# Kernel optimization log

Hardware: AMD Instinct MI355X
Metric: run time of the kernel (lower is better)

The kernel has to match this reference:

```python
import jax, jax.numpy as jnp
import numpy as np

B, C, H, W = 8, 512, 64, 64
KD, VD, OD = 64, 512, 512
BN_EPS = 1e-5


def setup_inputs() -> dict:
    key = jax.random.key(0)
    ks = jax.random.split(key, 10)
    s = lambda fan_in: 1.0 / np.sqrt(fan_in)
    return {
        "x": jax.random.normal(ks[0], (B, C, H, W), jnp.float32),
        "Wq": jax.random.normal(ks[1], (KD, C), jnp.float32) * s(C),
        "bq": jnp.zeros((KD,), jnp.float32),
        "Wk": jax.random.normal(ks[2], (KD, C), jnp.float32) * s(C),
        "bk": jnp.zeros((KD,), jnp.float32),
        "Wv": jax.random.normal(ks[3], (VD, C), jnp.float32) * s(C),
        "bv": jnp.zeros((VD,), jnp.float32),
        "gamma": jnp.zeros((1,), jnp.float32),  # torch init: zeros(1)
        "Wf": jax.random.normal(ks[4], (OD, VD), jnp.float32) * s(VD),
        "bn_w": jnp.ones((OD,), jnp.float32),
        "bn_b": jnp.zeros((OD,), jnp.float32),
        "bn_mean": jnp.zeros((OD,), jnp.float32),
        "bn_var": jnp.ones((OD,), jnp.float32),
    }


def reference(x, Wq, bq, Wk, bk, Wv, bv, gamma, Wf, bn_w, bn_b, bn_mean, bn_var):
    b, c, h, w = x.shape
    n = h * w
    # 1x1 convs == per-pixel channel matmuls
    q = jnp.einsum('bchw,kc->bkhw', x, Wq) + bq[None, :, None, None]  # [B,KD,H,W]
    k = jnp.einsum('bchw,kc->bkhw', x, Wk) + bk[None, :, None, None]
    v = jnp.einsum('bchw,vc->bvhw', x, Wv) + bv[None, :, None, None]
    q = q.reshape(b, -1, n)  # [B,KD,N]
    k = k.reshape(b, -1, n)
    v = v.reshape(b, -1, n)  # [B,VD,N]
    # energy[b, i, j] = q[:, :, i] . k[:, :, j]   (proj_query permuted)
    energy = jnp.einsum('bki,bkj->bij', q, k)  # [B,N,N]
    attention = jax.nn.softmax(energy, axis=-1)
    # out = value @ attention^T : out[b, v, i] = sum_j value[b, v, j] * attention[b, i, j]
    out = jnp.einsum('bvj,bij->bvi', v, attention)  # [B,VD,N]
    out = out.reshape(b, c, h, w)
    out = gamma * out + x
    # fuse: 1x1 conv (no bias) -> BatchNorm (inference) -> ReLU
    fused = jnp.einsum('bchw,oc->bohw', out, Wf)
    inv = jax.lax.rsqrt(bn_var + BN_EPS)
    fused = (fused - bn_mean[None, :, None, None]) * (bn_w * inv)[None, :, None, None] + bn_b[None, :, None, None]
    return jax.nn.relu(fused)
```

## Files before the change

### kernel.cpp

```cpp
#include <hip/hip_runtime.h>
#include <hip/hip_bf16.h>

typedef unsigned short u16;
typedef unsigned int u32;
typedef __attribute__((ext_vector_type(8))) short bf16x8;
typedef __attribute__((ext_vector_type(4))) float f32x4;
typedef __attribute__((ext_vector_type(4))) u16 u16x4;

#define B_ 8
#define C_ 512
#define N_ 4096
#define KD_ 64
#define VD_ 512
#define OD_ 512

static __device__ __forceinline__ float bf2f(u16 u) {
    union { u32 i; float f; } z; z.i = ((u32)u) << 16; return z.f;
}
static __device__ __forceinline__ u16 f2bf(float f) {
    union { float f; u32 u; } v; v.f = f;
    u32 r = v.u + 0x7fffu + ((v.u >> 16) & 1u);
    return (u16)(r >> 16);
}
static __device__ __forceinline__ u32 pkbf(float lo, float hi) {
    u32 ul = __float_as_uint(lo) + 0x8000u;
    u32 uh = __float_as_uint(hi) + 0x8000u;
    return __builtin_amdgcn_perm(uh, ul, 0x07060302u);
}
static __device__ __forceinline__ int swz(int row) { return ((row >> 2) + (row >> 4)) & 3; }

static __device__ __forceinline__ void tile_barrier() {
    asm volatile("s_waitcnt lgkmcnt(0)" ::: "memory");
    __builtin_amdgcn_s_barrier();
    asm volatile("" ::: "memory");
}

__global__ __launch_bounds__(256) void transpose_convert_kernel(
    const float* __restrict__ x, const float* __restrict__ Wf,
    const float* __restrict__ gamma,
    u16* __restrict__ xT, u16* __restrict__ Wf16)
{
    const int t = threadIdx.x;
    if (blockIdx.x >= 256) {
        const int tid = (blockIdx.x - 256) * 256 + t;
        const float4* src = (const float4*)Wf + (size_t)tid * 16;
        u16* dst = Wf16 + (size_t)tid * 64;
        #pragma unroll
        for (int j = 0; j < 16; j++) {
            const float4 f = src[j];
            u16x4 p;
            p[0] = f2bf(f.x); p[1] = f2bf(f.y); p[2] = f2bf(f.z); p[3] = f2bf(f.w);
            *(u16x4*)(dst + j * 4) = p;
        }
        return;
    }
    if (gamma[0] == 0.0f) return;
    __shared__ u32 tile[64][33];
    for (int it = 0; it < 16; it++) {
        const int bid = it * 256 + blockIdx.x;
        const int nt = bid & 63;
        const int ct = (bid >> 6) & 7;
        const int b  = bid >> 9;
        const float* xb  = x  + ((size_t)b * C_ + ct * 64) * N_ + nt * 64;
        u16*         xTb = xT + ((size_t)b * N_ + nt * 64) * C_ + ct * 64;
        {
            const int p  = t >> 3;
            const int n8 = t & 7;
            const float* r0 = xb + (size_t)(2 * p)     * N_ + n8 * 8;
            const float* r1 = xb + (size_t)(2 * p + 1) * N_ + n8 * 8;
            const float4 a0 = *(const float4*)(r0);
            const float4 a1 = *(const float4*)(r0 + 4);
            const float4 c0 = *(const float4*)(r1);
            const float4 c1 = *(const float4*)(r1 + 4);
            const float av[8] = { a0.x, a0.y, a0.z, a0.w, a1.x, a1.y, a1.z, a1.w };
            const float cv[8] = { c0.x, c0.y, c0.z, c0.w, c1.x, c1.y, c1.z, c1.w };
            #pragma unroll
            for (int j = 0; j < 8; j++)
                tile[n8 * 8 + j][p] = (u32)f2bf(av[j]) | ((u32)f2bf(cv[j]) << 16);
        }
        __syncthreads();
        #pragma unroll
        for (int h = 0; h < 2; h++) {
            const int id = t + h * 256;
            const int n  = id >> 3;
            const int q  = id & 7;
            uint4 val;
            val.x = tile[n][q * 4 + 0];
            val.y = tile[n][q * 4 + 1];
            val.z = tile[n][q * 4 + 2];
            val.w = tile[n][q * 4 + 3];
            *(uint4*)(xTb + (size_t)n * C_ + q * 8) = val;
        }
        __syncthreads();
    }
}

__global__ __launch_bounds__(256) void proj_kernel(
    const u16* __restrict__ xT,
    const float* __restrict__ Wq, const float* __restrict__ bq,
    const float* __restrict__ Wk, const float* __restrict__ bk,
    const float* __restrict__ Wv, const float* __restrict__ bv,
    const float* __restrict__ gamma,
    u16* __restrict__ q, u16* __restrict__ k, u16* __restrict__ v)
{
    if (gamma[0] == 0.0f) return;
    for (int it = 0; it < 2; it++) {
        const int bid = it * 256 + blockIdx.x;
        const int b = bid >> 6;
        const int p = (bid & 63) * 64 + (threadIdx.x & 63);
        const int dg = threadIdx.x >> 6;
        const u16* xrow = xT + ((size_t)b * N_ + p) * C_;
        for (int d0 = dg * 160; d0 < dg * 160 + 160; d0++) {
            const float* wrow; float bias; u16* dst; int dd; int dim;
            if (d0 < 64)       { dd = d0;       wrow = Wq + (size_t)dd * C_; bias = bq[dd]; dst = q; dim = KD_; }
            else if (d0 < 128) { dd = d0 - 64;  wrow = Wk + (size_t)dd * C_; bias = bk[dd]; dst = k; dim = KD_; }
            else               { dd = d0 - 128; wrow = Wv + (size_t)dd * C_; bias = bv[dd]; dst = v; dim = VD_; }
            float s = bias;
            for (int c = 0; c < C_; c++) s += bf2f(xrow[c]) * wrow[c];
            dst[((size_t)b * dim + dd) * N_ + p] = f2bf(s);
        }
    }
}

__global__ __launch_bounds__(256) void attn_kernel(
    const u16* __restrict__ xT, const u16* __restrict__ q,
    const u16* __restrict__ k, const u16* __restrict__ v,
    const float* __restrict__ gamma, u16* __restrict__ yT)
{
    const float g = gamma[0];
    if (g == 0.0f) return;
    __shared__ float pls[4][64];
    const int wv = threadIdx.x >> 6, lane = threadIdx.x & 63;
    for (int it = 0; it < 4; it++) {
        const int bid = it * 256 + blockIdx.x;
        const int b  = bid >> 7;
        const int q0 = (bid & 127) * 32 + wv * 8;
        const u16* kb = k + (size_t)b * KD_ * N_;
        const u16* vb = v + (size_t)b * VD_ * N_;
        for (int qi = 0; qi < 8; qi++) {
            const int i = q0 + qi;
            const float qv = bf2f(q[((size_t)b * KD_ + lane) * N_ + i]);
            float mx = -1e30f, l = 0.f;
            for (int jb = 0; jb < N_; jb += 64) {
                float e = 0.f;
                for (int kd = 0; kd < 64; kd++)
                    e += __shfl(qv, kd) * bf2f(kb[(size_t)kd * N_ + jb + lane]);
                const float nm = fmaxf(mx, e);
                l = l * __expf(mx - nm) + __expf(e - nm);
                mx = nm;
            }
            for (int off = 32; off; off >>= 1) {
                const float mo = __shfl_xor(mx, off);
                const float lo = __shfl_xor(l, off);
                const float nm = fmaxf(mx, mo);
                l = l * __expf(mx - nm) + lo * __expf(mo - nm);
                mx = nm;
            }
            float oacc[8];
            #pragma unroll
            for (int r = 0; r < 8; r++) oacc[r] = 0.f;
            for (int jb = 0; jb < N_; jb += 64) {
                float e = 0.f;
                for (int kd = 0; kd < 64; kd++)
                    e += __shfl(qv, kd) * bf2f(kb[(size_t)kd * N_ + jb + lane]);
                __syncthreads();
                pls[wv][lane] = __expf(e - mx);
                __syncthreads();
                for (int jj = 0; jj < 64; jj++) {
                    const float p = pls[wv][jj];
                    #pragma unroll
                    for (int r = 0; r < 8; r++)
                        oacc[r] += p * bf2f(vb[(size_t)(r * 64 + lane) * N_ + jb + jj]);
                }
            }
            const float inv = 1.f / l;
            #pragma unroll
            for (int r = 0; r < 8; r++) {
                const size_t idx = ((size_t)b * N_ + i) * C_ + r * 64 + lane;
                yT[idx] = f2bf(g * oacc[r] * inv + bf2f(xT[idx]));
            }
        }
    }
}

__global__ __launch_bounds__(256, 4) void gemm_bn_relu(
    const float* __restrict__ x, const u16* __restrict__ yT,
    const u16* __restrict__ Wf16, const float* __restrict__ gamma,
    const float* __restrict__ bnw, const float* __restrict__ bnb,
    const float* __restrict__ bnm, const float* __restrict__ bnv,
    float* __restrict__ out)
{
    __shared__ u16 lds_x[2][128 * 32];
    __shared__ u16 lds_w[2][64 * 32];

    const int bid = blockIdx.x;
    const int ot  = (bid >> 3) & 7;
    const int ptg = ((bid >> 6) << 3) | (bid & 7);
    const int b   = ptg >> 5;
    const int pt  = ptg & 31;

    const int t = threadIdx.x;
    const int lane = t & 63;
    const int wv = t >> 6;
    const int wm = wv >> 1;
    const int wn = wv & 1;
    const int lcol = lane & 15;
    const int kq = lane >> 4;

    const int rw = t >> 2, posw = t & 3;
    const int qlw = (posw - swz(rw)) & 3;
    const u16* Wsrc = Wf16 + (size_t)(ot * 64 + rw) * C_ + qlw * 8;
    const int wla = rw * 32 + posw * 8;

    int aaddr[4], baddr[2];
    #pragma unroll
    for (int i = 0; i < 4; i++) {
        const int P = wm * 64 + i * 16 + lcol;
        aaddr[i] = P * 32 + ((kq + swz(P)) & 3) * 8;
    }
    #pragma unroll
    for (int i = 0; i < 2; i++) {
        const int R = wn * 32 + i * 16 + lcol;
        baddr[i] = R * 32 + ((kq + swz(R)) & 3) * 8;
    }

    f32x4 acc[4][2];
    #pragma unroll
    for (int i = 0; i < 4; i++)
        #pragma unroll
        for (int j = 0; j < 2; j++)
            acc[i][j] = (f32x4){0.f, 0.f, 0.f, 0.f};

    auto compute = [&](int buf) {
        bf16x8 af[4], bfg[2];
        #pragma unroll
        for (int mi = 0; mi < 4; mi++)
            af[mi] = *(const bf16x8*)&lds_x[buf][aaddr[mi]];
        #pragma unroll
        for (int ni = 0; ni < 2; ni++)
            bfg[ni] = *(const bf16x8*)&lds_w[buf][baddr[ni]];
        #pragma unroll
        for (int mi = 0; mi < 4; mi++)
            #pragma unroll
            for (int ni = 0; ni < 2; ni++)
                acc[mi][ni] = __builtin_amdgcn_mfma_f32_16x16x32_bf16(
                    af[mi], bfg[ni], acc[mi][ni], 0, 0, 0);
    };

    if (gamma[0] == 0.0f) {
        const int pq = t & 15;
        const int c2 = t >> 4;
        const float* xe = x + ((size_t)b * C_ + 2 * c2) * N_ + pt * 128 + pq * 4;
        const float* xo = xe + N_;
        int xidx[2][4];
        #pragma unroll
        for (int qd = 0; qd < 2; qd++)
            #pragma unroll
            for (int i = 0; i < 4; i++) {
                const int p = pq * 4 + qd * 64 + i;
                xidx[qd][i] = p * 16 + (((c2 >> 2) + swz(p)) & 3) * 4 + (c2 & 3);
            }
        float4 e0A, e1A, o0A, o1A, e0B, e1B, o0B, o1B;
        uint4 wA, wB;
        auto loadA = [&](int ks) {
            const float* pe = xe + (size_t)ks * 32 * N_;
            const float* po = xo + (size_t)ks * 32 * N_;
            e0A = *(const float4*)pe; e1A = *(const float4*)(pe + 64);
            o0A = *(const float4*)po; o1A = *(const float4*)(po + 64);
            wA = *(const uint4*)(Wsrc + ks * 32);
        };
        auto loadB = [&](int ks) {
            const float* pe = xe + (size_t)ks * 32 * N_;
            const float* po = xo + (size_t)ks * 32 * N_;
            e0B = *(const float4*)pe; e1B = *(const float4*)(pe + 64);
            o0B = *(const float4*)po; o1B = *(const float4*)(po + 64);
            wB = *(const uint4*)(Wsrc + ks * 32);
        };
        auto writeA = [&](int buf) {
            u32* lx = (u32*)lds_x[buf];
            lx[xidx[0][0]] = pkbf(e0A.x, o0A.x);
            lx[xidx[0][1]] = pkbf(e0A.y, o0A.y);
            lx[xidx[0][2]] = pkbf(e0A.z, o0A.z);
            lx[xidx[0][3]] = pkbf(e0A.w, o0A.w);
            lx[xidx[1][0]] = pkbf(e1A.x, o1A.x);
            lx[xidx[1][1]] = pkbf(e1A.y, o1A.y);
            lx[xidx[1][2]] = pkbf(e1A.z, o1A.z);
            lx[xidx[1][3]] = pkbf(e1A.w, o1A.w);
            *(uint4*)&lds_w[buf][wla] = wA;
        };
        auto writeB = [&](int buf) {
            u32* lx = (u32*)lds_x[buf];
            lx[xidx[0][0]] = pkbf(e0B.x, o0B.x);
            lx[xidx[0][1]] = pkbf(e0B.y, o0B.y);
            lx[xidx[0][2]] = pkbf(e0B.z, o0B.z);
            lx[xidx[0][3]] = pkbf(e0B.w, o0B.w);
            lx[xidx[1][0]] = pkbf(e1B.x, o1B.x);
            lx[xidx[1][1]] = pkbf(e1B.y, o1B.y);
            lx[xidx[1][2]] = pkbf(e1B.z, o1B.z);
            lx[xidx[1][3]] = pkbf(e1B.w, o1B.w);
            *(uint4*)&lds_w[buf][wla] = wB;
        };

        loadA(0); loadB(1);
        writeA(0);
        for (int ks = 0; ks < 16; ks += 2) {
            tile_barrier();
            if (ks + 2 < 16) loadA(ks + 2);
            compute(0);
            writeB(1);
            tile_barrier();
            if (ks + 3 < 16) loadB(ks + 3);
            compute(1);
            if (ks + 2 < 16) writeA(0);
        }
    } else {
        const int ry = t >> 1;
        const int pd0 = (t & 1) * 2;
        const int qy0 = (pd0 - swz(ry)) & 3;
        const int qy1 = (pd0 + 1 - swz(ry)) & 3;
        const u16* Ysrc = yT + ((size_t)b * N_ + pt * 128 + ry) * C_;
        const int yla = ry * 32 + pd0 * 8;
        uint4 y0A, y1A, y0B, y1B, wA, wB;
        auto loadA = [&](int ks) {
            y0A = *(const uint4*)(Ysrc + ks * 32 + qy0 * 8);
            y1A = *(const uint4*)(Ysrc + ks * 32 + qy1 * 8);
            wA  = *(const uint4*)(Wsrc + ks * 32);
        };
        auto loadB = [&](int ks) {
            y0B = *(const uint4*)(Ysrc + ks * 32 + qy0 * 8);
            y1B = *(const uint4*)(Ysrc + ks * 32 + qy1 * 8);
            wB  = *(const uint4*)(Wsrc + ks * 32);
        };
        auto writeA = [&](int buf) {
            *(uint4*)&lds_x[buf][yla] = y0A;
            *(uint4*)&lds_x[buf][yla + 8] = y1A;
            *(uint4*)&lds_w[buf][wla] = wA;
        };
        auto writeB = [&](int buf) {
            *(uint4*)&lds_x[buf][yla] = y0B;
            *(uint4*)&lds_x[buf][yla + 8] = y1B;
            *(uint4*)&lds_w[buf][wla] = wB;
        };

        loadA(0); loadB(1);
        writeA(0);
        for (int ks = 0; ks < 16; ks += 2) {
            tile_barrier();
            if (ks + 2 < 16) loadA(ks + 2);
            compute(0);
            writeB(1);
            tile_barrier();
            if (ks + 3 < 16) loadB(ks + 3);
            compute(1);
            if (ks + 2 < 16) writeA(0);
        }
    }

    float scale[2], shift[2];
    #pragma unroll
    for (int ni = 0; ni < 2; ni++) {
        const int o = ot * 64 + wn * 32 + ni * 16 + lcol;
        const float s = bnw[o] * rsqrtf(bnv[o] + 1e-5f);
        scale[ni] = s;
        shift[ni] = bnb[o] - bnm[o] * s;
    }
    #pragma unroll
    for (int mi = 0; mi < 4; mi++) {
        const int npix = pt * 128 + wm * 64 + mi * 16 + kq * 4;
        #pragma unroll
        for (int ni = 0; ni < 2; ni++) {
            const int o = ot * 64 + wn * 32 + ni * 16 + lcol;
            f32x4 pk;
            #pragma unroll
            for (int r = 0; r < 4; r++)
                pk[r] = fmaxf(acc[mi][ni][r] * scale[ni] + shift[ni], 0.0f);
            *(f32x4*)(out + ((size_t)b * OD_ + o) * N_ + npix) = pk;
        }
    }
}

extern "C" void kernel_launch(void* const* d_in, const int* in_sizes, int n_in,
                              void* d_out, int out_size, void* d_ws, size_t ws_size,
                              hipStream_t stream) {
    const float* x     = (const float*)d_in[0];
    const float* Wq    = (const float*)d_in[1];
    const float* bq    = (const float*)d_in[2];
    const float* Wk    = (const float*)d_in[3];
    const float* bk    = (const float*)d_in[4];
    const float* Wv    = (const float*)d_in[5];
    const float* bv    = (const float*)d_in[6];
    const float* gamma = (const float*)d_in[7];
    const float* Wf    = (const float*)d_in[8];
    const float* bnw   = (const float*)d_in[9];
    const float* bnb   = (const float*)d_in[10];
    const float* bnm   = (const float*)d_in[11];
    const float* bnv   = (const float*)d_in[12];
    float* out = (float*)d_out;

    char* ws = (char*)d_ws;
    u16* Wf16 = (u16*)(ws);
    u16* xT   = (u16*)(ws + 524288);
    u16* yT   = (u16*)(ws + 34078720);
    u16* q    = (u16*)(ws + 67633152);
    u16* k    = (u16*)(ws + 71827456);
    u16* v    = (u16*)(ws + 76021760);

    transpose_convert_kernel<<<272, 256, 0, stream>>>(x, Wf, gamma, xT, Wf16);
    proj_kernel<<<256, 256, 0, stream>>>(xT, Wq, bq, Wk, bk, Wv, bv, gamma, q, k, v);
    attn_kernel<<<256, 256, 0, stream>>>(xT, q, k, v, gamma, yT);
    gemm_bn_relu<<<2048, 256, 0, stream>>>(x, yT, Wf16, gamma, bnw, bnb, bnm, bnv, out);
}
```

Before: 172.7 us.

## Enlarge final GEMM tile to 128x128 output channels and set MFMA priority

The fused 1x1-conv/BN/ReLU GEMM now computes 128 output channels per block instead of 64, which halves the grid and doubles the MFMA work done per LDS load. The gamma==0 path changes x loading from float4 vectors to strided scalar loads so the thread-to-pixel mapping matches the new tile. MFMA sections are wrapped in s_setprio. The intent is to cut redundant reads of x, which are now shared across twice as many output channels. The cost is more accumulator registers and twice the weight LDS, which may reduce occupancy under launch_bounds(256,4).

```diff
diff --git a/kernel.cpp b/kernel.cpp
--- a/kernel.cpp
+++ b/kernel.cpp
@@ -191,13 +191,14 @@
     float* __restrict__ out)
 {
     __shared__ u16 lds_x[2][128 * 32];
-    __shared__ u16 lds_w[2][64 * 32];
+    __shared__ u16 lds_w[2][128 * 32];
 
     const int bid = blockIdx.x;
-    const int ot  = (bid >> 3) & 7;
-    const int ptg = ((bid >> 6) << 3) | (bid & 7);
-    const int b   = ptg >> 5;
-    const int pt  = ptg & 31;
+    const int pt8 = bid & 7;
+    const int ot  = (bid >> 3) & 3;
+    const int g   = bid >> 5;
+    const int pt  = (g & 3) * 8 + pt8;
+    const int b   = g >> 2;
 
     const int t = threadIdx.x;
     const int lane = t & 63;
@@ -208,97 +209,88 @@
     const int kq = lane >> 4;
 
     const int rw = t >> 2, posw = t & 3;
-    const int qlw = (posw - swz(rw)) & 3;
-    const u16* Wsrc = Wf16 + (size_t)(ot * 64 + rw) * C_ + qlw * 8;
-    const int wla = rw * 32 + posw * 8;
-
-    int aaddr[4], baddr[2];
+    const int ql = (posw - swz(rw)) & 3;
+    const u16* WT0 = Wf16 + (size_t)(ot * 128 + rw) * C_ + ql * 8;
+    const u16* WT1 = WT0 + (size_t)64 * C_;
+    const int wla0 = rw * 32 + posw * 8;
+    const int wla1 = wla0 + 64 * 32;
+
+    int aaddr[4], baddr[4];
     #pragma unroll
     for (int i = 0; i < 4; i++) {
         const int P = wm * 64 + i * 16 + lcol;
         aaddr[i] = P * 32 + ((kq + swz(P)) & 3) * 8;
-    }
-    #pragma unroll
-    for (int i = 0; i < 2; i++) {
-        const int R = wn * 32 + i * 16 + lcol;
+        const int R = wn * 64 + i * 16 + lcol;
         baddr[i] = R * 32 + ((kq + swz(R)) & 3) * 8;
     }
 
-    f32x4 acc[4][2];
+    f32x4 acc[4][4];
     #pragma unroll
     for (int i = 0; i < 4; i++)
         #pragma unroll
-        for (int j = 0; j < 2; j++)
+        for (int j = 0; j < 4; j++)
             acc[i][j] = (f32x4){0.f, 0.f, 0.f, 0.f};
 
     auto compute = [&](int buf) {
-        bf16x8 af[4], bfg[2];
+        bf16x8 af[4], bfg[4];
         #pragma unroll
         for (int mi = 0; mi < 4; mi++)
             af[mi] = *(const bf16x8*)&lds_x[buf][aaddr[mi]];
         #pragma unroll
-        for (int ni = 0; ni < 2; ni++)
+        for (int ni = 0; ni < 4; ni++)
             bfg[ni] = *(const bf16x8*)&lds_w[buf][baddr[ni]];
+        __builtin_amdgcn_s_setprio(1);
         #pragma unroll
         for (int mi = 0; mi < 4; mi++)
             #pragma unroll
-            for (int ni = 0; ni < 2; ni++)
+            for (int ni = 0; ni < 4; ni++)
                 acc[mi][ni] = __builtin_amdgcn_mfma_f32_16x16x32_bf16(
                     af[mi], bfg[ni], acc[mi][ni], 0, 0, 0);
+        __builtin_amdgcn_s_setprio(0);
     };
 
     if (gamma[0] == 0.0f) {
-        const int pq = t & 15;
-        const int c2 = t >> 4;
-        const float* xe = x + ((size_t)b * C_ + 2 * c2) * N_ + pt * 128 + pq * 4;
-        const float* xo = xe + N_;
-        int xidx[2][4];
-        #pragma unroll
-        for (int qd = 0; qd < 2; qd++)
-            #pragma unroll
-            for (int i = 0; i < 4; i++) {
-                const int p = pq * 4 + qd * 64 + i;
-                xidx[qd][i] = p * 16 + (((c2 >> 2) + swz(p)) & 3) * 4 + (c2 & 3);
-            }
-        float4 e0A, e1A, o0A, o1A, e0B, e1B, o0B, o1B;
-        uint4 wA, wB;
+        const int q4 = t & 15, cp = t >> 4;
+        int xidx[8];
+        #pragma unroll
+        for (int j = 0; j < 8; j++) {
+            const int p = q4 + 16 * j;
+            xidx[j] = p * 16 + (((cp >> 2) + swz(p)) & 3) * 4 + (cp & 3);
+        }
+        const float* eptr = x + ((size_t)b * C_ + 2 * cp) * N_ + pt * 128 + q4;
+        const float* optr = eptr + N_;
+
+        float eA_[8], oA_[8], eB_[8], oB_[8];
+        uint4 wA0, wA1, wB0, wB1;
         auto loadA = [&](int ks) {
-            const float* pe = xe + (size_t)ks * 32 * N_;
-            const float* po = xo + (size_t)ks * 32 * N_;
-            e0A = *(const float4*)pe; e1A = *(const float4*)(pe + 64);
-            o0A = *(const float4*)po; o1A = *(const float4*)(po + 64);
-            wA = *(const uint4*)(Wsrc + ks * 32);
+            const float* ee = eptr + (size_t)ks * 32 * N_;
+            const float* oo = optr + (size_t)ks * 32 * N_;
+            #pragma unroll
+            for (int j = 0; j < 8; j++) { eA_[j] = ee[16 * j]; oA_[j] = oo[16 * j]; }
+            wA0 = *(const uint4*)(WT0 + ks * 32);
+            wA1 = *(const uint4*)(WT1 + ks * 32);
         };
         auto loadB = [&](int ks) {
-            const float* pe = xe + (size_t)ks * 32 * N_;
-            const float* po = xo + (size_t)ks * 32 * N_;
-            e0B = *(const float4*)pe; e1B = *(const float4*)(pe + 64);
-            o0B = *(const float4*)po; o1B = *(const float4*)(po + 64);
-            wB = *(const uint4*)(Wsrc + ks * 32);
+            const float* ee = eptr + (size_t)ks * 32 * N_;
+            const float* oo = optr + (size_t)ks * 32 * N_;
+            #pragma unroll
+            for (int j = 0; j < 8; j++) { eB_[j] = ee[16 * j]; oB_[j] = oo[16 * j]; }
+            wB0 = *(const uint4*)(WT0 + ks * 32);
+            wB1 = *(const uint4*)(WT1 + ks * 32);
         };
         auto writeA = [&](int buf) {
             u32* lx = (u32*)lds_x[buf];
-            lx[xidx[0][0]] = pkbf(e0A.x, o0A.x);
-            lx[xidx[0][1]] = pkbf(e0A.y, o0A.y);
-            lx[xidx[0][2]] = pkbf(e0A.z, o0A.z);
-            lx[xidx[0][3]] = pkbf(e0A.w, o0A.w);
-            lx[xidx[1][0]] = pkbf(e1A.x, o1A.x);
-            lx[xidx[1][1]] = pkbf(e1A.y, o1A.y);
-            lx[xidx[1][2]] = pkbf(e1A.z, o1A.z);
-            lx[xidx[1][3]] = pkbf(e1A.w, o1A.w);
-            *(uint4*)&lds_w[buf][wla] = wA;
+            #pragma unroll
+            for (int j = 0; j < 8; j++) lx[xidx[j]] = pkbf(eA_[j], oA_[j]);
+            *(uint4*)&lds_w[buf][wla0] = wA0;
+            *(uint4*)&lds_w[buf][wla1] = wA1;
         };
         auto writeB = [&](int buf) {
             u32* lx = (u32*)lds_x[buf];
-            lx[xidx[0][0]] = pkbf(e0B.x, o0B.x);
-            lx[xidx[0][1]] = pkbf(e0B.y, o0B.y);
-            lx[xidx[0][2]] = pkbf(e0B.z, o0B.z);
-            lx[xidx[0][3]] = pkbf(e0B.w, o0B.w);
-            lx[xidx[1][0]] = pkbf(e1B.x, o1B.x);
-            lx[xidx[1][1]] = pkbf(e1B.y, o1B.y);
-            lx[xidx[1][2]] = pkbf(e1B.z, o1B.z);
-            lx[xidx[1][3]] = pkbf(e1B.w, o1B.w);
-            *(uint4*)&lds_w[buf][wla] = wB;
+            #pragma unroll
+            for (int j = 0; j < 8; j++) lx[xidx[j]] = pkbf(eB_[j], oB_[j]);
+            *(uint4*)&lds_w[buf][wla0] = wB0;
+            *(uint4*)&lds_w[buf][wla1] = wB1;
         };
 
         loadA(0); loadB(1);
@@ -314,32 +306,32 @@
             if (ks + 2 < 16) writeA(0);
         }
     } else {
-        const int ry = t >> 1;
-        const int pd0 = (t & 1) * 2;
-        const int qy0 = (pd0 - swz(ry)) & 3;
-        const int qy1 = (pd0 + 1 - swz(ry)) & 3;
-        const u16* Ysrc = yT + ((size_t)b * N_ + pt * 128 + ry) * C_;
-        const int yla = ry * 32 + pd0 * 8;
-        uint4 y0A, y1A, y0B, y1B, wA, wB;
+        const u16* YT0 = yT + ((size_t)b * N_ + pt * 128 + rw) * C_ + ql * 8;
+        const u16* YT1 = YT0 + (size_t)64 * C_;
+        uint4 yA0, yA1, yB0, yB1, wA0, wA1, wB0, wB1;
         auto loadA = [&](int ks) {
-            y0A = *(const uint4*)(Ysrc + ks * 32 + qy0 * 8);
-            y1A = *(const uint4*)(Ysrc + ks * 32 + qy1 * 8);
-            wA  = *(const uint4*)(Wsrc + ks * 32);
+            yA0 = *(const uint4*)(YT0 + ks * 32);
+            yA1 = *(const uint4*)(YT1 + ks * 32);
+            wA0 = *(const uint4*)(WT0 + ks * 32);
+            wA1 = *(const uint4*)(WT1 + ks * 32);
         };
         auto loadB = [&](int ks) {
-            y0B = *(const uint4*)(Ysrc + ks * 32 + qy0 * 8);
-            y1B = *(const uint4*)(Ysrc + ks * 32 + qy1 * 8);
-            wB  = *(const uint4*)(Wsrc + ks * 32);
+            yB0 = *(const uint4*)(YT0 + ks * 32);
+            yB1 = *(const uint4*)(YT1 + ks * 32);
+            wB0 = *(const uint4*)(WT0 + ks * 32);
+            wB1 = *(const uint4*)(WT1 + ks * 32);
         };
         auto writeA = [&](int buf) {
-            *(uint4*)&lds_x[buf][yla] = y0A;
-            *(uint4*)&lds_x[buf][yla + 8] = y1A;
-            *(uint4*)&lds_w[buf][wla] = wA;
+            *(uint4*)&lds_x[buf][wla0] = yA0;
+            *(uint4*)&lds_x[buf][wla1] = yA1;
+            *(uint4*)&lds_w[buf][wla0] = wA0;
+            *(uint4*)&lds_w[buf][wla1] = wA1;
         };
         auto writeB = [&](int buf) {
-            *(uint4*)&lds_x[buf][yla] = y0B;
-            *(uint4*)&lds_x[buf][yla + 8] = y1B;
-            *(uint4*)&lds_w[buf][wla] = wB;
+            *(uint4*)&lds_x[buf][wla0] = yB0;
+            *(uint4*)&lds_x[buf][wla1] = yB1;
+            *(uint4*)&lds_w[buf][wla0] = wB0;
+            *(uint4*)&lds_w[buf][wla1] = wB1;
         };
 
         loadA(0); loadB(1);
@@ -356,10 +348,10 @@
         }
     }
 
-    float scale[2], shift[2];
+    float scale[4], shift[4];
     #pragma unroll
-    for (int ni = 0; ni < 2; ni++) {
-        const int o = ot * 64 + wn * 32 + ni * 16 + lcol;
+    for (int ni = 0; ni < 4; ni++) {
+        const int o = ot * 128 + wn * 64 + ni * 16 + lcol;
         const float s = bnw[o] * rsqrtf(bnv[o] + 1e-5f);
         scale[ni] = s;
         shift[ni] = bnb[o] - bnm[o] * s;
@@ -368,8 +360,8 @@
     for (int mi = 0; mi < 4; mi++) {
         const int npix = pt * 128 + wm * 64 + mi * 16 + kq * 4;
         #pragma unroll
-        for (int ni = 0; ni < 2; ni++) {
-            const int o = ot * 64 + wn * 32 + ni * 16 + lcol;
+        for (int ni = 0; ni < 4; ni++) {
+            const int o = ot * 128 + wn * 64 + ni * 16 + lcol;
             f32x4 pk;
             #pragma unroll
             for (int r = 0; r < 4; r++)
@@ -408,5 +400,5 @@
     transpose_convert_kernel<<<272, 256, 0, stream>>>(x, Wf, gamma, xT, Wf16);
     proj_kernel<<<256, 256, 0, stream>>>(xT, Wq, bq, Wk, bk, Wv, bv, gamma, q, k, v);
     attn_kernel<<<256, 256, 0, stream>>>(xT, q, k, v, gamma, yT);
-    gemm_bn_relu<<<2048, 256, 0, stream>>>(x, yT, Wf16, gamma, bnw, bnb, bnm, bnv, out);
-}
+    gemm_bn_relu<<<1024, 256, 0, stream>>>(x, yT, Wf16, gamma, bnw, bnb, bnm, bnv, out);
+}
```

Result: slower. 320.1 us (+85.3%).
